# Kernel tuning notes

Measured on AMD Instinct MI355X. Metric: run time of the kernel, lower is better.

The kernel has to match this reference:

```python
import jax, jax.numpy as jnp
import numpy as np

IN_F = 4096
OUT_F = 4096
GROUP = 8
N_GROUPS = OUT_F * IN_F // GROUP  # 2097152
BATCH = 32


def _dequant_3bit(weight_q3, weight_norm):
    # weight_q3: [G, 3] bytes (stored int32, values 0..255)
    # weight_norm: [G, 1] fp16 per-group abs-max scale
    p = weight_q3.astype(jnp.int32)
    val = p[:, 0] | (p[:, 1] << 8) | (p[:, 2] << 16)          # [G] 24-bit word
    shifts = jnp.arange(GROUP, dtype=jnp.int32) * 3           # [8]
    q = ((val[:, None] >> shifts[None, :]) & 7).astype(jnp.float32)  # [G, 8] in {0..7}
    n = weight_norm.astype(jnp.float32)                        # [G, 1]
    w = (q / 7.0) * (2.0 * n) - n                              # de-normalize to [-n, n]
    return w.reshape(OUT_F, IN_F)


def setup_inputs() -> dict:
    key = jax.random.key(0)
    k1, k2, k3, k4 = jax.random.split(key, 4)
    x = jax.random.normal(k1, (BATCH, IN_F), dtype=jnp.float32)
    weight_q3 = jax.random.randint(k2, (N_GROUPS, 3), 0, 256, dtype=jnp.int32)
    weight_norm = jax.random.uniform(k3, (N_GROUPS, 1), dtype=jnp.float16, minval=0.01, maxval=1.0)
    bias = jax.random.normal(k4, (OUT_F,), dtype=jnp.float32)
    return {"x": x, "weight_q3": weight_q3, "weight_norm": weight_norm, "bias": bias}


def reference(x, weight_q3, weight_norm, bias):
    w = _dequant_3bit(weight_q3, weight_norm)  # [OUT_F, IN_F] fp32
    return x @ w.T + bias                      # F.linear semantics
```

## Files before the change

### kernel.cpp

```cpp
#include <hip/hip_runtime.h>
#include <hip/hip_fp16.h>

#define IN_F   4096
#define OUT_F  4096
#define BATCH  32
#define NGPR   512
#define BN     16
#define NW     8
#define QPITCH 516
#define NPITCH 516

typedef float f32x4  __attribute__((ext_vector_type(4)));
typedef short short8 __attribute__((ext_vector_type(8)));

__device__ __forceinline__ unsigned short f2bf_u(float f) {
    return __builtin_bit_cast(unsigned short, (__bf16)f);
}

__global__ __launch_bounds__(512)
void pack_x_kernel(const float* __restrict__ x, unsigned short* __restrict__ apk)
{
    const int tau = blockIdx.x * 512 + threadIdx.x;
    const int row = tau >> 9;
    const int c   = tau & 511;
    const float4 lo = *reinterpret_cast<const float4*>(&x[row * IN_F + c * 8]);
    const float4 hi = *reinterpret_cast<const float4*>(&x[row * IN_F + c * 8 + 4]);
    union { unsigned short us[8]; uint4 v; } pk;
    pk.us[0] = f2bf_u(lo.x); pk.us[1] = f2bf_u(lo.y);
    pk.us[2] = f2bf_u(lo.z); pk.us[3] = f2bf_u(lo.w);
    pk.us[4] = f2bf_u(hi.x); pk.us[5] = f2bf_u(hi.y);
    pk.us[6] = f2bf_u(hi.z); pk.us[7] = f2bf_u(hi.w);
    const int a = row >> 4, cl = row & 15, s = c >> 2, q = c & 3;
    const int unit = (a * 128 + s) * 64 + q * 16 + cl;
    *reinterpret_cast<uint4*>(&apk[unit * 8]) = pk.v;
}

template<bool PACKED>
__global__ __launch_bounds__(512, 2)
void l3b_main(const float* __restrict__ x,
              const int* __restrict__ wq3,
              const void* __restrict__ wnorm_raw,
              const float* __restrict__ bias,
              float* __restrict__ out,
              const unsigned short* __restrict__ apk)
{
    __shared__ unsigned int qw[BN][QPITCH];
    __shared__ float        nrm[BN][NPITCH];
    __shared__ float        red[NW][BATCH][17];

    const int tid   = threadIdx.x;
    const int w     = tid >> 6;
    const int lane  = tid & 63;
    const int nbase = blockIdx.x * BN;

    const int q  = lane >> 4;
    const int cl = lane & 15;

    const unsigned short* wn16  = (const unsigned short*)wnorm_raw;
    const float*          wn32  = (const float*)wnorm_raw;
    const unsigned int*   wnu32 = (const unsigned int*)wnorm_raw;
    int mode;
    {
        const unsigned short h = wn16[lane];
        const float v16 = __half2float(__builtin_bit_cast(__half, h));
        const float vbf = __builtin_bit_cast(float, (unsigned int)h << 16);
        const float v32 = wn32[lane];
        const int c16 = __popcll(__ballot(v16 > 0.0095f && v16 < 1.0005f));
        const int cbf = __popcll(__ballot(vbf > 0.0095f && vbf < 1.0005f));
        const int c32 = __popcll(__ballot(v32 > 0.0095f && v32 < 1.0005f));
        if (c16 >= c32 && c16 >= cbf) {
            mode = 1;
        } else if (c32 > cbf + 8) {
            mode = 0;
        } else if (cbf > c32 + 8) {
            mode = 2;
        } else {
            const int z = __popcll(__ballot((wnu32[lane] & 0x1FFFu) == 0u));
            mode = (z >= 48) ? 0 : 2;
        }
    }

    {
        const int* qbase = wq3 + (long)nbase * (NGPR * 3);
        #pragma unroll
        for (int r2 = 0; r2 < 4; ++r2) {
            const int o = r2 * 6144 + tid * 12;
            const int4 ia = *reinterpret_cast<const int4*>(qbase + o);
            const int4 ib = *reinterpret_cast<const int4*>(qbase + o + 4);
            const int4 ic = *reinterpret_cast<const int4*>(qbase + o + 8);
            uint4 wd;
            wd.x = (unsigned)(ia.x | (ia.y << 8) | (ia.z << 16));
            wd.y = (unsigned)(ia.w | (ib.x << 8) | (ib.y << 16));
            wd.z = (unsigned)(ib.z | (ib.w << 8) | (ic.x << 16));
            wd.w = (unsigned)(ic.y | (ic.z << 8) | (ic.w << 16));
            const int row = r2 * 4 + (tid >> 7);
            const int col = (tid * 4) & 511;
            *reinterpret_cast<uint4*>(&qw[row][col]) = wd;
        }
    }

    if (mode == 0) {
        const float* nb = wn32 + (long)nbase * NGPR;
        #pragma unroll
        for (int j = 0; j < 4; ++j) {
            const int e = j * 2048 + tid * 4;
            const float4 v = *reinterpret_cast<const float4*>(nb + e);
            *reinterpret_cast<float4*>(&nrm[e >> 9][e & 511]) = v;
        }
    } else {
        const unsigned short* nb = wn16 + (long)nbase * NGPR;
        #pragma unroll
        for (int j = 0; j < 4; ++j) {
            const int e = j * 2048 + tid * 4;
            const ushort4 v = *reinterpret_cast<const ushort4*>(nb + e);
            float4 f;
            if (mode == 1) {
                f.x = __half2float(__builtin_bit_cast(__half, v.x));
                f.y = __half2float(__builtin_bit_cast(__half, v.y));
                f.z = __half2float(__builtin_bit_cast(__half, v.z));
                f.w = __half2float(__builtin_bit_cast(__half, v.w));
            } else {
                f.x = __builtin_bit_cast(float, (unsigned int)v.x << 16);
                f.y = __builtin_bit_cast(float, (unsigned int)v.y << 16);
                f.z = __builtin_bit_cast(float, (unsigned int)v.z << 16);
                f.w = __builtin_bit_cast(float, (unsigned int)v.w << 16);
            }
            *reinterpret_cast<float4*>(&nrm[e >> 9][e & 511]) = f;
        }
    }

    __syncthreads();

    f32x4 acc0 = {0.f, 0.f, 0.f, 0.f};
    f32x4 acc1 = {0.f, 0.f, 0.f, 0.f};
    const int s0 = w * 16;

    #pragma unroll 4
    for (int i = 0; i < 16; ++i) {
        const int s = s0 + i;
        const int g = s * 4 + q;

        const unsigned int qv = qw[cl][g];
        const float n  = nrm[cl][g];
        const float av = n * 0.285714285714285714f;
        union { unsigned short us[8]; short8 v; } B;
        #pragma unroll
        for (int e = 0; e < 8; ++e) {
            const float qf = (float)((qv >> (3 * e)) & 7u);
            B.us[e] = f2bf_u(fmaf(qf, av, -n));
        }

        short8 A0, A1;
        if (PACKED) {
            A0 = *reinterpret_cast<const short8*>(&apk[(s * 64 + lane) * 8]);
            A1 = *reinterpret_cast<const short8*>(&apk[((128 + s) * 64 + lane) * 8]);
        } else {
            const int kg = s * 32 + q * 8;
            const float4 a0lo = *reinterpret_cast<const float4*>(&x[cl        * IN_F + kg]);
            const float4 a0hi = *reinterpret_cast<const float4*>(&x[cl        * IN_F + kg + 4]);
            const float4 a1lo = *reinterpret_cast<const float4*>(&x[(cl + 16) * IN_F + kg]);
            const float4 a1hi = *reinterpret_cast<const float4*>(&x[(cl + 16) * IN_F + kg + 4]);
            union { unsigned short us[8]; short8 v; } U0, U1;
            U0.us[0] = f2bf_u(a0lo.x); U0.us[1] = f2bf_u(a0lo.y);
            U0.us[2] = f2bf_u(a0lo.z); U0.us[3] = f2bf_u(a0lo.w);
            U0.us[4] = f2bf_u(a0hi.x); U0.us[5] = f2bf_u(a0hi.y);
            U0.us[6] = f2bf_u(a0hi.z); U0.us[7] = f2bf_u(a0hi.w);
            U1.us[0] = f2bf_u(a1lo.x); U1.us[1] = f2bf_u(a1lo.y);
            U1.us[2] = f2bf_u(a1lo.z); U1.us[3] = f2bf_u(a1lo.w);
            U1.us[4] = f2bf_u(a1hi.x); U1.us[5] = f2bf_u(a1hi.y);
            U1.us[6] = f2bf_u(a1hi.z); U1.us[7] = f2bf_u(a1hi.w);
            A0 = U0.v; A1 = U1.v;
        }

        acc0 = __builtin_amdgcn_mfma_f32_16x16x32_bf16(A0, B.v, acc0, 0, 0, 0);
        acc1 = __builtin_amdgcn_mfma_f32_16x16x32_bf16(A1, B.v, acc1, 0, 0, 0);
    }

    #pragma unroll
    for (int i = 0; i < 4; ++i) {
        red[w][q * 4 + i][cl]      = acc0[i];
        red[w][16 + q * 4 + i][cl] = acc1[i];
    }
    __syncthreads();
    {
        const int m  = tid >> 4;
        const int nl = tid & 15;
        float ssum = 0.f;
        #pragma unroll
        for (int wv = 0; wv < NW; ++wv) ssum += red[wv][m][nl];
        out[m * OUT_F + nbase + nl] = ssum + bias[nbase + nl];
    }
}

extern "C" void kernel_launch(void* const* d_in, const int* in_sizes, int n_in,
                              void* d_out, int out_size, void* d_ws, size_t ws_size,
                              hipStream_t stream) {
    const float* x    = (const float*)d_in[0];
    const int*   wq3  = (const int*)d_in[1];
    const void*  wn   = (const void*)d_in[2];
    const float* bias = (const float*)d_in[3];
    float*       out  = (float*)d_out;

    if (ws_size >= (size_t)(2 * 128 * 64 * 8 * 2)) {
        unsigned short* apk = (unsigned short*)d_ws;
        pack_x_kernel<<<dim3(32), dim3(512), 0, stream>>>(x, apk);
        l3b_main<true><<<dim3(OUT_F / BN), dim3(512), 0, stream>>>(x, wq3, wn, bias, out, apk);
    } else {
        l3b_main<false><<<dim3(OUT_F / BN), dim3(512), 0, stream>>>(x, wq3, wn, bias, out, nullptr);
    }
}
```

Before: 16.81 us.

## Load weights via direct global-to-LDS DMA in two halves overlapping compute

Replaces the register-staged load, byte-pack and store of quantized weights and norms with global_load_lds 16-byte transfers straight into shared memory. The raw int32 bytes and fp16 norms are kept as-is and decoded at use time. The K range is split into two halves with partial vmcnt waits, so compute on the first half overlaps the loading of the second. The pack kernel also moves to smaller blocks. This raises LDS footprint (96KB for weights), which may reduce occupancy, and relies on hand-written waitcnt counts being correct.

Result: slower. 22.46 us (+33.6%).

```diff
diff --git a/kernel.cpp b/kernel.cpp
--- a/kernel.cpp
+++ b/kernel.cpp
@@ -7,8 +7,6 @@
 #define NGPR   512
 #define BN     16
 #define NW     8
-#define QPITCH 516
-#define NPITCH 516
 
 typedef float f32x4  __attribute__((ext_vector_type(4)));
 typedef short short8 __attribute__((ext_vector_type(8)));
@@ -17,10 +15,16 @@
     return __builtin_bit_cast(unsigned short, (__bf16)f);
 }
 
-__global__ __launch_bounds__(512)
+__device__ __forceinline__ void gload16(const void* gsrc, void* lds) {
+    __builtin_amdgcn_global_load_lds(
+        (const __attribute__((address_space(1))) void*)gsrc,
+        (__attribute__((address_space(3))) void*)lds, 16, 0, 0);
+}
+
+__global__ __launch_bounds__(128)
 void pack_x_kernel(const float* __restrict__ x, unsigned short* __restrict__ apk)
 {
-    const int tau = blockIdx.x * 512 + threadIdx.x;
+    const int tau = blockIdx.x * 128 + threadIdx.x;
     const int row = tau >> 9;
     const int c   = tau & 511;
     const float4 lo = *reinterpret_cast<const float4*>(&x[row * IN_F + c * 8]);
@@ -44,9 +48,9 @@
               float* __restrict__ out,
               const unsigned short* __restrict__ apk)
 {
-    __shared__ unsigned int qw[BN][QPITCH];
-    __shared__ float        nrm[BN][NPITCH];
-    __shared__ float        red[NW][BATCH][17];
+    __shared__ unsigned int qls[24576];
+    __shared__ unsigned int nls[8192];
+    __shared__ float red[NW][BATCH][17];
 
     const int tid   = threadIdx.x;
     const int w     = tid >> 6;
@@ -80,73 +84,67 @@
         }
     }
 
-    {
-        const int* qbase = wq3 + (long)nbase * (NGPR * 3);
-        #pragma unroll
-        for (int r2 = 0; r2 < 4; ++r2) {
-            const int o = r2 * 6144 + tid * 12;
-            const int4 ia = *reinterpret_cast<const int4*>(qbase + o);
-            const int4 ib = *reinterpret_cast<const int4*>(qbase + o + 4);
-            const int4 ic = *reinterpret_cast<const int4*>(qbase + o + 8);
-            uint4 wd;
-            wd.x = (unsigned)(ia.x | (ia.y << 8) | (ia.z << 16));
-            wd.y = (unsigned)(ia.w | (ib.x << 8) | (ib.y << 16));
-            wd.z = (unsigned)(ib.z | (ib.w << 8) | (ic.x << 16));
-            wd.w = (unsigned)(ic.y | (ic.z << 8) | (ic.w << 16));
-            const int row = r2 * 4 + (tid >> 7);
-            const int col = (tid * 4) & 511;
-            *reinterpret_cast<uint4*>(&qw[row][col]) = wd;
-        }
-    }
-
+    const int* qgbase = wq3 + (long)nbase * 1536;
+    #pragma unroll
+    for (int j = 0; j < 6; ++j) {
+        const int B = j * 512 + tid;
+        gload16(qgbase + (B & 15) * 1536 + (B >> 4) * 4, &qls[B * 4]);
+    }
     if (mode == 0) {
         const float* nb = wn32 + (long)nbase * NGPR;
         #pragma unroll
-        for (int j = 0; j < 4; ++j) {
-            const int e = j * 2048 + tid * 4;
-            const float4 v = *reinterpret_cast<const float4*>(nb + e);
-            *reinterpret_cast<float4*>(&nrm[e >> 9][e & 511]) = v;
+        for (int j = 0; j < 2; ++j) {
+            const int B = j * 512 + tid;
+            gload16(nb + (B & 15) * 512 + (B >> 4) * 4, &nls[B * 4]);
         }
     } else {
         const unsigned short* nb = wn16 + (long)nbase * NGPR;
-        #pragma unroll
-        for (int j = 0; j < 4; ++j) {
-            const int e = j * 2048 + tid * 4;
-            const ushort4 v = *reinterpret_cast<const ushort4*>(nb + e);
-            float4 f;
-            if (mode == 1) {
-                f.x = __half2float(__builtin_bit_cast(__half, v.x));
-                f.y = __half2float(__builtin_bit_cast(__half, v.y));
-                f.z = __half2float(__builtin_bit_cast(__half, v.z));
-                f.w = __half2float(__builtin_bit_cast(__half, v.w));
-            } else {
-                f.x = __builtin_bit_cast(float, (unsigned int)v.x << 16);
-                f.y = __builtin_bit_cast(float, (unsigned int)v.y << 16);
-                f.z = __builtin_bit_cast(float, (unsigned int)v.z << 16);
-                f.w = __builtin_bit_cast(float, (unsigned int)v.w << 16);
-            }
-            *reinterpret_cast<float4*>(&nrm[e >> 9][e & 511]) = f;
-        }
-    }
-
-    __syncthreads();
+        const int B = tid;
+        gload16(nb + (B & 15) * 512 + (B >> 4) * 8, (unsigned short*)nls + B * 8);
+    }
+    #pragma unroll
+    for (int j = 6; j < 12; ++j) {
+        const int B = j * 512 + tid;
+        gload16(qgbase + (B & 15) * 1536 + (B >> 4) * 4, &qls[B * 4]);
+    }
+    if (mode == 0) {
+        const float* nb = wn32 + (long)nbase * NGPR;
+        #pragma unroll
+        for (int j = 2; j < 4; ++j) {
+            const int B = j * 512 + tid;
+            gload16(nb + (B & 15) * 512 + (B >> 4) * 4, &nls[B * 4]);
+        }
+    } else {
+        const unsigned short* nb = wn16 + (long)nbase * NGPR;
+        const int B = 512 + tid;
+        gload16(nb + (B & 15) * 512 + (B >> 4) * 8, (unsigned short*)nls + B * 8);
+    }
 
     f32x4 acc0 = {0.f, 0.f, 0.f, 0.f};
     f32x4 acc1 = {0.f, 0.f, 0.f, 0.f};
-    const int s0 = w * 16;
-
-    #pragma unroll 4
-    for (int i = 0; i < 16; ++i) {
-        const int s = s0 + i;
-        const int g = s * 4 + q;
-
-        const unsigned int qv = qw[cl][g];
-        const float n  = nrm[cl][g];
+
+    auto body = [&](int s) {
+        const int g  = s * 4 + q;
+        const int b0 = g * 12;
+        const unsigned p0 = qls[(( b0      >> 4) << 6) + (cl << 2) + (( b0       & 15) >> 2)];
+        const unsigned p1 = qls[(((b0 + 4) >> 4) << 6) + (cl << 2) + (((b0 + 4)  & 15) >> 2)];
+        const unsigned p2 = qls[(((b0 + 8) >> 4) << 6) + (cl << 2) + (((b0 + 8)  & 15) >> 2)];
+        const unsigned val = (p0 & 0xFFu) | ((p1 & 0xFFu) << 8) | ((p2 & 0xFFu) << 16);
+
+        float n;
+        if (mode == 0) {
+            n = ((const float*)nls)[((g >> 2) << 6) + (cl << 2) + (g & 3)];
+        } else {
+            const unsigned short u =
+                ((const unsigned short*)nls)[((g >> 3) << 7) + (cl << 3) + (g & 7)];
+            n = (mode == 1) ? __half2float(__builtin_bit_cast(__half, u))
+                            : __builtin_bit_cast(float, (unsigned)u << 16);
+        }
         const float av = n * 0.285714285714285714f;
         union { unsigned short us[8]; short8 v; } B;
         #pragma unroll
         for (int e = 0; e < 8; ++e) {
-            const float qf = (float)((qv >> (3 * e)) & 7u);
+            const float qf = (float)((val >> (3 * e)) & 7u);
             B.us[e] = f2bf_u(fmaf(qf, av, -n));
         }
 
@@ -174,7 +172,20 @@
 
         acc0 = __builtin_amdgcn_mfma_f32_16x16x32_bf16(A0, B.v, acc0, 0, 0, 0);
         acc1 = __builtin_amdgcn_mfma_f32_16x16x32_bf16(A1, B.v, acc1, 0, 0, 0);
-    }
+    };
+
+    if (mode == 0) asm volatile("s_waitcnt vmcnt(8)" ::: "memory");
+    else           asm volatile("s_waitcnt vmcnt(7)" ::: "memory");
+    __builtin_amdgcn_s_barrier();
+
+    #pragma unroll 4
+    for (int i = 0; i < 8; ++i) body(w * 8 + i);
+
+    asm volatile("s_waitcnt vmcnt(0)" ::: "memory");
+    __builtin_amdgcn_s_barrier();
+
+    #pragma unroll 4
+    for (int i = 0; i < 8; ++i) body(64 + w * 8 + i);
 
     #pragma unroll
     for (int i = 0; i < 4; ++i) {
@@ -203,7 +214,7 @@
 
     if (ws_size >= (size_t)(2 * 128 * 64 * 8 * 2)) {
         unsigned short* apk = (unsigned short*)d_ws;
-        pack_x_kernel<<<dim3(32), dim3(512), 0, stream>>>(x, apk);
+        pack_x_kernel<<<dim3(128), dim3(128), 0, stream>>>(x, apk);
         l3b_main<true><<<dim3(OUT_F / BN), dim3(512), 0, stream>>>(x, wq3, wn, bias, out, apk);
     } else {
         l3b_main<false><<<dim3(OUT_F / BN), dim3(512), 0, stream>>>(x, wq3, wn, bias, out, nullptr);
```

## Split K across two blocks per output tile with atomic accumulation

Applied to the files above, without the earlier changes.

Each 16-column output tile is now handled by two 256-thread blocks, each covering half of the K dimension. This doubles the grid to 512 blocks and halves the shared-memory footprint per block, aiming at better occupancy and load balance across CUs. Partial sums are combined with float atomicAdd into an output zeroed by an added memset, and the bias is added only by the first half. The cost is an extra memset launch, atomic traffic, and a summation order that is no longer deterministic.

Result: slower. 19.80 us (+17.8%).

```diff
diff --git a/kernel.cpp b/kernel.cpp
--- a/kernel.cpp
+++ b/kernel.cpp
@@ -6,9 +6,9 @@
 #define BATCH  32
 #define NGPR   512
 #define BN     16
-#define NW     8
-#define QPITCH 516
-#define NPITCH 516
+#define NW     4
+#define QP     260
+#define NP     260
 
 typedef float f32x4  __attribute__((ext_vector_type(4)));
 typedef short short8 __attribute__((ext_vector_type(8)));
@@ -17,10 +17,10 @@
     return __builtin_bit_cast(unsigned short, (__bf16)f);
 }
 
-__global__ __launch_bounds__(512)
+__global__ __launch_bounds__(256)
 void pack_x_kernel(const float* __restrict__ x, unsigned short* __restrict__ apk)
 {
-    const int tau = blockIdx.x * 512 + threadIdx.x;
+    const int tau = blockIdx.x * 256 + threadIdx.x;
     const int row = tau >> 9;
     const int c   = tau & 511;
     const float4 lo = *reinterpret_cast<const float4*>(&x[row * IN_F + c * 8]);
@@ -36,7 +36,7 @@
 }
 
 template<bool PACKED>
-__global__ __launch_bounds__(512, 2)
+__global__ __launch_bounds__(256, 3)
 void l3b_main(const float* __restrict__ x,
               const int* __restrict__ wq3,
               const void* __restrict__ wnorm_raw,
@@ -44,14 +44,15 @@
               float* __restrict__ out,
               const unsigned short* __restrict__ apk)
 {
-    __shared__ unsigned int qw[BN][QPITCH];
-    __shared__ float        nrm[BN][NPITCH];
+    __shared__ unsigned int qw[BN][QP];
+    __shared__ float        nrm[BN][NP];
     __shared__ float        red[NW][BATCH][17];
 
     const int tid   = threadIdx.x;
     const int w     = tid >> 6;
     const int lane  = tid & 63;
-    const int nbase = blockIdx.x * BN;
+    const int nbase = (blockIdx.x >> 1) * BN;
+    const int kh    = blockIdx.x & 1;
 
     const int q  = lane >> 4;
     const int cl = lane & 15;
@@ -80,52 +81,64 @@
         }
     }
 
+    if (mode == 0) {
+        const float* nb = wn32 + (long)nbase * NGPR + kh * 256;
+        #pragma unroll
+        for (int j = 0; j < 4; ++j) {
+            const int e = j * 1024 + tid * 4;
+            const int row = e >> 8, col = e & 255;
+            const float4 v = *reinterpret_cast<const float4*>(nb + (long)row * NGPR + col);
+            *reinterpret_cast<float4*>(&nrm[row][col]) = v;
+        }
+    } else {
+        const unsigned short* nb = wn16 + (long)nbase * NGPR + kh * 256;
+        #pragma unroll
+        for (int j = 0; j < 2; ++j) {
+            const int e = j * 2048 + tid * 8;
+            const int row = e >> 8, col = e & 255;
+            union { unsigned short us[8]; uint4 v; } u;
+            u.v = *reinterpret_cast<const uint4*>(nb + (long)row * NGPR + col);
+            float4 f0, f1;
+            if (mode == 1) {
+                f0.x = __half2float(__builtin_bit_cast(__half, u.us[0]));
+                f0.y = __half2float(__builtin_bit_cast(__half, u.us[1]));
+                f0.z = __half2float(__builtin_bit_cast(__half, u.us[2]));
+                f0.w = __half2float(__builtin_bit_cast(__half, u.us[3]));
+                f1.x = __half2float(__builtin_bit_cast(__half, u.us[4]));
+                f1.y = __half2float(__builtin_bit_cast(__half, u.us[5]));
+                f1.z = __half2float(__builtin_bit_cast(__half, u.us[6]));
+                f1.w = __half2float(__builtin_bit_cast(__half, u.us[7]));
+            } else {
+                f0.x = __builtin_bit_cast(float, (unsigned)u.us[0] << 16);
+                f0.y = __builtin_bit_cast(float, (unsigned)u.us[1] << 16);
+                f0.z = __builtin_bit_cast(float, (unsigned)u.us[2] << 16);
+                f0.w = __builtin_bit_cast(float, (unsigned)u.us[3] << 16);
+                f1.x = __builtin_bit_cast(float, (unsigned)u.us[4] << 16);
+                f1.y = __builtin_bit_cast(float, (unsigned)u.us[5] << 16);
+                f1.z = __builtin_bit_cast(float, (unsigned)u.us[6] << 16);
+                f1.w = __builtin_bit_cast(float, (unsigned)u.us[7] << 16);
+            }
+            *reinterpret_cast<float4*>(&nrm[row][col])     = f0;
+            *reinterpret_cast<float4*>(&nrm[row][col + 4]) = f1;
+        }
+    }
+
     {
-        const int* qbase = wq3 + (long)nbase * (NGPR * 3);
+        const int* qgbase = wq3 + (long)nbase * 1536 + kh * 768;
         #pragma unroll
         for (int r2 = 0; r2 < 4; ++r2) {
-            const int o = r2 * 6144 + tid * 12;
-            const int4 ia = *reinterpret_cast<const int4*>(qbase + o);
-            const int4 ib = *reinterpret_cast<const int4*>(qbase + o + 4);
-            const int4 ic = *reinterpret_cast<const int4*>(qbase + o + 8);
+            const int row = r2 * 4 + (tid >> 6);
+            const int cb  = (tid & 63) * 12;
+            const int* p = qgbase + (long)row * 1536 + cb;
+            const int4 ia = *reinterpret_cast<const int4*>(p);
+            const int4 ib = *reinterpret_cast<const int4*>(p + 4);
+            const int4 ic = *reinterpret_cast<const int4*>(p + 8);
             uint4 wd;
             wd.x = (unsigned)(ia.x | (ia.y << 8) | (ia.z << 16));
             wd.y = (unsigned)(ia.w | (ib.x << 8) | (ib.y << 16));
             wd.z = (unsigned)(ib.z | (ib.w << 8) | (ic.x << 16));
             wd.w = (unsigned)(ic.y | (ic.z << 8) | (ic.w << 16));
-            const int row = r2 * 4 + (tid >> 7);
-            const int col = (tid * 4) & 511;
-            *reinterpret_cast<uint4*>(&qw[row][col]) = wd;
-        }
-    }
-
-    if (mode == 0) {
-        const float* nb = wn32 + (long)nbase * NGPR;
-        #pragma unroll
-        for (int j = 0; j < 4; ++j) {
-            const int e = j * 2048 + tid * 4;
-            const float4 v = *reinterpret_cast<const float4*>(nb + e);
-            *reinterpret_cast<float4*>(&nrm[e >> 9][e & 511]) = v;
-        }
-    } else {
-        const unsigned short* nb = wn16 + (long)nbase * NGPR;
-        #pragma unroll
-        for (int j = 0; j < 4; ++j) {
-            const int e = j * 2048 + tid * 4;
-            const ushort4 v = *reinterpret_cast<const ushort4*>(nb + e);
-            float4 f;
-            if (mode == 1) {
-                f.x = __half2float(__builtin_bit_cast(__half, v.x));
-                f.y = __half2float(__builtin_bit_cast(__half, v.y));
-                f.z = __half2float(__builtin_bit_cast(__half, v.z));
-                f.w = __half2float(__builtin_bit_cast(__half, v.w));
-            } else {
-                f.x = __builtin_bit_cast(float, (unsigned int)v.x << 16);
-                f.y = __builtin_bit_cast(float, (unsigned int)v.y << 16);
-                f.z = __builtin_bit_cast(float, (unsigned int)v.z << 16);
-                f.w = __builtin_bit_cast(float, (unsigned int)v.w << 16);
-            }
-            *reinterpret_cast<float4*>(&nrm[e >> 9][e & 511]) = f;
+            *reinterpret_cast<uint4*>(&qw[row][(tid & 63) * 4]) = wd;
         }
     }
 
@@ -133,11 +146,10 @@
 
     f32x4 acc0 = {0.f, 0.f, 0.f, 0.f};
     f32x4 acc1 = {0.f, 0.f, 0.f, 0.f};
-    const int s0 = w * 16;
 
     #pragma unroll 4
     for (int i = 0; i < 16; ++i) {
-        const int s = s0 + i;
+        const int s = w * 16 + i;
         const int g = s * 4 + q;
 
         const unsigned int qv = qw[cl][g];
@@ -150,12 +162,13 @@
             B.us[e] = f2bf_u(fmaf(qf, av, -n));
         }
 
+        const int sg = kh * 64 + s;
         short8 A0, A1;
         if (PACKED) {
-            A0 = *reinterpret_cast<const short8*>(&apk[(s * 64 + lane) * 8]);
-            A1 = *reinterpret_cast<const short8*>(&apk[((128 + s) * 64 + lane) * 8]);
+            A0 = *reinterpret_cast<const short8*>(&apk[(sg * 64 + lane) * 8]);
+            A1 = *reinterpret_cast<const short8*>(&apk[((128 + sg) * 64 + lane) * 8]);
         } else {
-            const int kg = s * 32 + q * 8;
+            const int kg = sg * 32 + q * 8;
             const float4 a0lo = *reinterpret_cast<const float4*>(&x[cl        * IN_F + kg]);
             const float4 a0hi = *reinterpret_cast<const float4*>(&x[cl        * IN_F + kg + 4]);
             const float4 a1lo = *reinterpret_cast<const float4*>(&x[(cl + 16) * IN_F + kg]);
@@ -185,10 +198,15 @@
     {
         const int m  = tid >> 4;
         const int nl = tid & 15;
-        float ssum = 0.f;
-        #pragma unroll
-        for (int wv = 0; wv < NW; ++wv) ssum += red[wv][m][nl];
-        out[m * OUT_F + nbase + nl] = ssum + bias[nbase + nl];
+        float s1 = 0.f, s2 = 0.f;
+        #pragma unroll
+        for (int wv = 0; wv < NW; ++wv) {
+            s1 += red[wv][m][nl];
+            s2 += red[wv][m + 16][nl];
+        }
+        const float b = (kh == 0) ? bias[nbase + nl] : 0.0f;
+        atomicAdd(&out[m * OUT_F + nbase + nl], s1 + b);
+        atomicAdd(&out[(m + 16) * OUT_F + nbase + nl], s2 + b);
     }
 }
 
@@ -201,11 +219,13 @@
     const float* bias = (const float*)d_in[3];
     float*       out  = (float*)d_out;
 
+    hipMemsetAsync(d_out, 0, (size_t)BATCH * OUT_F * sizeof(float), stream);
+
     if (ws_size >= (size_t)(2 * 128 * 64 * 8 * 2)) {
         unsigned short* apk = (unsigned short*)d_ws;
-        pack_x_kernel<<<dim3(32), dim3(512), 0, stream>>>(x, apk);
-        l3b_main<true><<<dim3(OUT_F / BN), dim3(512), 0, stream>>>(x, wq3, wn, bias, out, apk);
+        pack_x_kernel<<<dim3(64), dim3(256), 0, stream>>>(x, apk);
+        l3b_main<true><<<dim3(512), dim3(256), 0, stream>>>(x, wq3, wn, bias, out, apk);
     } else {
-        l3b_main<false><<<dim3(OUT_F / BN), dim3(512), 0, stream>>>(x, wq3, wn, bias, out, nullptr);
-    }
-}
+        l3b_main<false><<<dim3(512), dim3(256), 0, stream>>>(x, wq3, wn, bias, out, nullptr);
+    }
+}
```
